# Optimization experiments

Measured on AMD Instinct MI355X. Metric: run time of the kernel, lower is better.

The kernel has to match this reference:

```python
import jax, jax.numpy as jnp
import numpy as np

N, E = 100000, 1600000
IN, EDGE_DIM, HID, OUT, HEADS = 128, 16, 32, 32, 2


def _glorot(key, shape, scale=0.1):
    return jax.random.normal(key, shape, dtype=jnp.float32) * scale


def setup_inputs() -> dict:
    key = jax.random.key(0)
    ks = jax.random.split(key, 20)
    HC1 = HEADS * HID
    return {
        "x": jax.random.normal(ks[0], (N, IN), dtype=jnp.float32),
        "edge_index": jax.random.randint(ks[1], (2, E), 0, N, dtype=jnp.int32),
        "edge_attr": jax.random.normal(ks[2], (E, EDGE_DIM), dtype=jnp.float32),
        # layer 1 (heads=HEADS, concat=True)
        "W1l": _glorot(ks[3], (IN, HC1)), "b1l": jnp.zeros((HC1,), jnp.float32),
        "W1r": _glorot(ks[4], (IN, HC1)), "b1r": jnp.zeros((HC1,), jnp.float32),
        "W1e": _glorot(ks[5], (EDGE_DIM, HC1)),
        "att1": _glorot(ks[6], (HEADS, HID)),
        "bias1": jnp.zeros((HC1,), jnp.float32),
        # layer 2 (heads=1, concat=False)
        "W2l": _glorot(ks[7], (HC1, HID)), "b2l": jnp.zeros((HID,), jnp.float32),
        "W2r": _glorot(ks[8], (HC1, HID)), "b2r": jnp.zeros((HID,), jnp.float32),
        "W2e": _glorot(ks[9], (EDGE_DIM, HID)),
        "att2": _glorot(ks[10], (1, HID)),
        "bias2": jnp.zeros((HID,), jnp.float32),
        # final linear
        "Wlin": _glorot(ks[11], (HID, OUT)), "blin": jnp.zeros((OUT,), jnp.float32),
    }


def gatv2_layer(x, src, dst, edge_attr, Wl, bl, Wr, br, We, att, bias, H, C, concat):
    n = x.shape[0]
    xl = (x @ Wl + bl).reshape(n, H, C)   # source transform (lin_l)
    xr = (x @ Wr + br).reshape(n, H, C)   # target transform (lin_r)
    ea = (edge_attr @ We).reshape(-1, H, C)
    m = xl[src] + xr[dst] + ea                       # [E, H, C]
    e = jnp.sum(jax.nn.leaky_relu(m, 0.2) * att, axis=-1)  # [E, H]
    # segment softmax over incoming edges of each destination node
    emax = jax.ops.segment_max(e, dst, num_segments=n)
    emax = jnp.where(jnp.isfinite(emax), emax, 0.0)
    ee = jnp.exp(e - emax[dst])
    denom = jax.ops.segment_sum(ee, dst, num_segments=n)
    alpha = ee / (denom[dst] + 1e-16)                # [E, H]
    out = jax.ops.segment_sum(xl[src] * alpha[..., None], dst, num_segments=n)  # [N, H, C]
    out = out.reshape(n, H * C) if concat else out.mean(axis=1)
    return out + bias


def reference(x, edge_index, edge_attr, W1l, b1l, W1r, b1r, W1e, att1, bias1,
              W2l, b2l, W2r, b2r, W2e, att2, bias2, Wlin, blin):
    src, dst = edge_index[0], edge_index[1]
    h = jax.nn.elu(gatv2_layer(x, src, dst, edge_attr, W1l, b1l, W1r, b1r, W1e,
                               att1, bias1, HEADS, HID, True))
    h = jax.nn.elu(gatv2_layer(h, src, dst, edge_attr, W2l, b2l, W2r, b2r, W2e,
                               att2, bias2, 1, HID, False))
    return h @ Wlin + blin
```

## Files before the change

### kernel.cpp

```cpp
#include <hip/hip_runtime.h>
#include <hip/hip_fp16.h>
#include <cstdint>
#include <cstddef>


typedef _Float16 half8 __attribute__((ext_vector_type(8)));
typedef float f32x4 __attribute__((ext_vector_type(4)));

__global__ void hist_kernel(const int* __restrict__ dst, int* __restrict__ deg, int E) {
    int e = blockIdx.x * blockDim.x + threadIdx.x;
    if (e < E) atomicAdd(&deg[dst[e]], 1);
}

__global__ void scan_part(const int* __restrict__ deg, int* __restrict__ bsum, int n) {
    int tid = threadIdx.x;
    int base = blockIdx.x * 1024 + tid * 4;
    int s = 0;
#pragma unroll
    for (int j = 0; j < 4; ++j) {
        int i = base + j;
        if (i < n) s += deg[i];
    }
#pragma unroll
    for (int off = 1; off < 64; off <<= 1) s += __shfl_xor(s, off, 64);
    __shared__ int ws[4];
    if ((tid & 63) == 0) ws[tid >> 6] = s;
    __syncthreads();
    if (tid == 0) bsum[blockIdx.x] = ws[0] + ws[1] + ws[2] + ws[3];
}

__global__ void scan_mid(int* __restrict__ bsum, int* __restrict__ rowstart, int nb, int n) {
    int tid = threadIdx.x;
    int v = (tid < nb) ? bsum[tid] : 0;
    int incl = v;
#pragma unroll
    for (int off = 1; off < 64; off <<= 1) {
        int t = __shfl_up(incl, off, 64);
        if ((tid & 63) >= off) incl += t;
    }
    __shared__ int w0;
    if (tid == 63) w0 = incl;
    __syncthreads();
    if (tid >= 64) incl += w0;
    if (tid < nb) bsum[tid] = incl - v;
    if (tid == nb - 1) rowstart[n] = incl;
}

__global__ void scan_fin(const int* __restrict__ deg, const int* __restrict__ bsum,
                         int* __restrict__ rowstart, int n) {
    int tid = threadIdx.x;
    int lane = tid & 63, wid = tid >> 6;
    int base = blockIdx.x * 1024 + tid * 4;
    int v[4];
    int s = 0;
#pragma unroll
    for (int j = 0; j < 4; ++j) {
        int i = base + j;
        v[j] = (i < n) ? deg[i] : 0;
        s += v[j];
    }
    int incl = s;
#pragma unroll
    for (int off = 1; off < 64; off <<= 1) {
        int t = __shfl_up(incl, off, 64);
        if (lane >= off) incl += t;
    }
    __shared__ int ws[4];
    if (lane == 63) ws[wid] = incl;
    __syncthreads();
    int wofs = 0;
    for (int w2 = 0; w2 < wid; ++w2) wofs += ws[w2];
    int acc = bsum[blockIdx.x] + wofs + (incl - s);
#pragma unroll
    for (int j = 0; j < 4; ++j) {
        int i = base + j;
        if (i < n) rowstart[i] = acc;
        acc += v[j];
    }
}

template <int K, int Mh>
__device__ void wprep_body(int i, const float* __restrict__ Wl, const float* __restrict__ Wr,
                           __half* __restrict__ Wfrag) {
    constexpr int KS = K / 32;
    if (i >= K * 2 * Mh) return;
    int j = i & 7;
    int lane = (i >> 3) & 63;
    int rest = i >> 9;
    int ks = rest % KS;
    int nt = rest / KS;
    int k = ks * 32 + ((lane >> 4) & 3) * 8 + j;
    int col = nt * 16 + (lane & 15);
    float v = (col < Mh) ? Wl[k * Mh + col] : Wr[k * Mh + (col - Mh)];
    Wfrag[i] = __float2half(v);
}

__global__ void wprep_both(const float* W1l, const float* W1r, __half* Wf1,
                           const float* W2l, const float* W2r, __half* Wf2) {
    int bid = blockIdx.x;
    int tid = threadIdx.x;
    if (bid < 64) wprep_body<128, 64>(bid * 256 + tid, W1l, W1r, Wf1);
    else          wprep_body<64, 32>((bid - 64) * 256 + tid, W2l, W2r, Wf2);
}

template <int K, int Mh, int BM>
__device__ void gemm_body(int bid, __half* xs, const float* __restrict__ x,
                          const __half* __restrict__ Wfrag, const float* __restrict__ bl,
                          const float* __restrict__ br, __half* __restrict__ yl,
                          __half* __restrict__ yr, int n) {
    constexpr int KS = K / 32;
    constexpr int NT = (2 * Mh) / 16;
    constexpr int RW = BM / 64;
    constexpr int LDP = K + 8;
    int tid = threadIdx.x;
    int lane = tid & 63;
    int wave = tid >> 6;
    int node0 = bid * BM;
    constexpr int ITER = (BM * K) / (256 * 4);
#pragma unroll
    for (int it = 0; it < ITER; ++it) {
        int base = (it * 256 + tid) * 4;
        int row = base / K, kk = base % K;
        float4 v = make_float4(0.f, 0.f, 0.f, 0.f);
        if (node0 + row < n) v = *(const float4*)&x[(size_t)(node0 + row) * K + kk];
        __half2* d = (__half2*)&xs[row * LDP + kk];
        d[0] = __float22half2_rn(make_float2(v.x, v.y));
        d[1] = __float22half2_rn(make_float2(v.z, v.w));
    }
    __syncthreads();
    f32x4 acc[RW][NT];
#pragma unroll
    for (int r = 0; r < RW; ++r)
#pragma unroll
        for (int t = 0; t < NT; ++t) {
            f32x4 z = {0.f, 0.f, 0.f, 0.f};
            acc[r][t] = z;
        }
    int r0 = lane & 15, kof = (lane >> 4) * 8;
#pragma unroll
    for (int ks = 0; ks < KS; ++ks) {
        half8 a[RW];
#pragma unroll
        for (int r = 0; r < RW; ++r) {
            int row = (wave * RW + r) * 16 + r0;
            a[r] = *reinterpret_cast<const half8*>(&xs[row * LDP + ks * 32 + kof]);
        }
#pragma unroll
        for (int t = 0; t < NT; ++t) {
            half8 b = *reinterpret_cast<const half8*>(&Wfrag[(((size_t)t * KS + ks) * 64 + lane) * 8]);
#pragma unroll
            for (int r = 0; r < RW; ++r)
                acc[r][t] = __builtin_amdgcn_mfma_f32_16x16x32_f16(a[r], b, acc[r][t], 0, 0, 0);
        }
    }
#pragma unroll
    for (int r = 0; r < RW; ++r) {
#pragma unroll
        for (int t = 0; t < NT; ++t) {
            int col = t * 16 + (lane & 15);
            float bv = (col < Mh) ? bl[col] : br[col - Mh];
#pragma unroll
            for (int q = 0; q < 4; ++q) {
                int node = node0 + (wave * RW + r) * 16 + (lane >> 4) * 4 + q;
                if (node < n) {
                    float v = acc[r][t][q] + bv;
                    if (col < Mh) yl[(size_t)node * Mh + col] = __float2half(v);
                    else          yr[(size_t)node * Mh + (col - Mh)] = __float2half(v);
                }
            }
        }
    }
}

__device__ void scatter_body(int e, const int* __restrict__ src, const int* __restrict__ dst,
                             const float* __restrict__ eattr, const int* __restrict__ rowstart,
                             int* __restrict__ cursor, int2* __restrict__ es,
                             __half* __restrict__ eah, int E) {
    if (e < E) {
        int d = dst[e];
        int p = atomicAdd(&cursor[d], 1);
        es[rowstart[d] + p] = make_int2(e, src[e]);
        const float4* s4 = (const float4*)&eattr[(size_t)e * 16];
        float4 a = s4[0], b = s4[1], c = s4[2], f = s4[3];
        __half2 h[8];
        h[0] = __float22half2_rn(make_float2(a.x, a.y));
        h[1] = __float22half2_rn(make_float2(a.z, a.w));
        h[2] = __float22half2_rn(make_float2(b.x, b.y));
        h[3] = __float22half2_rn(make_float2(b.z, b.w));
        h[4] = __float22half2_rn(make_float2(c.x, c.y));
        h[5] = __float22half2_rn(make_float2(c.z, c.w));
        h[6] = __float22half2_rn(make_float2(f.x, f.y));
        h[7] = __float22half2_rn(make_float2(f.z, f.w));
        int4* o = (int4*)&eah[(size_t)e * 16];
        o[0] = *(int4*)&h[0];
        o[1] = *(int4*)&h[4];
    }
}

__device__ void dcount_body(int bid, int* h, const int* __restrict__ deg,
                            int* __restrict__ counts, int n) {
    int tid = threadIdx.x;
    h[tid] = 0;
    __syncthreads();
    int base = bid * 4096;
#pragma unroll
    for (int j = 0; j < 16; ++j) {
        int i = base + j * 256 + tid;
        if (i < n) {
            int b = deg[i];
            b = (b > 255) ? 255 : b;
            atomicAdd(&h[b], 1);
        }
    }
    __syncthreads();
    counts[bid * 256 + tid] = h[tid];
}

__global__ __launch_bounds__(256) void fat_kernel(
    int nbG, int nbS,
    const float* __restrict__ x, const __half* __restrict__ Wf1,
    const float* __restrict__ b1l, const float* __restrict__ b1r,
    __half* __restrict__ A, __half* __restrict__ B, int n,
    const int* __restrict__ src, const int* __restrict__ dst,
    const float* __restrict__ eattr, const int* __restrict__ rowstart,
    int* __restrict__ cursor, int2* __restrict__ es, __half* __restrict__ eah, int E,
    const int* __restrict__ deg, int* __restrict__ counts) {
    __shared__ __half xs[64 * 136];
    __shared__ int hcnt[256];
    int bid = blockIdx.x;
    if (bid < nbG) {
        gemm_body<128, 64, 64>(bid, xs, x, Wf1, b1l, b1r, A, B, n);
    } else if (bid < nbG + nbS) {
        scatter_body((bid - nbG) * 256 + threadIdx.x, src, dst, eattr, rowstart, cursor, es,
                     eah, E);
    } else {
        dcount_body(bid - nbG - nbS, hcnt, deg, counts, n);
    }
}

__global__ void dbase_kernel(const int* __restrict__ counts, int* __restrict__ base, int nblk) {
    int b = threadIdx.x;
    int tot = 0;
    for (int k = 0; k < nblk; ++k) tot += counts[k * 256 + b];
    __shared__ int ws[4];
    int lane = b & 63, wid = b >> 6;
    int incl = tot;
#pragma unroll
    for (int off = 1; off < 64; off <<= 1) {
        int t = __shfl_up(incl, off, 64);
        if (lane >= off) incl += t;
    }
    if (lane == 63) ws[wid] = incl;
    __syncthreads();
    int wofs = 0;
    for (int w = 0; w < wid; ++w) wofs += ws[w];
    int acc = wofs + incl - tot;
    for (int k = 0; k < nblk; ++k) {
        base[k * 256 + b] = acc;
        acc += counts[k * 256 + b];
    }
}

__global__ __launch_bounds__(256) void dscatter_block(const int* __restrict__ deg,
                                                      const int* __restrict__ base,
                                                      int* __restrict__ nodeperm, int n) {
    __shared__ int h[256];
    int tid = threadIdx.x;
    h[tid] = 0;
    __syncthreads();
    int bbase = blockIdx.x * 4096;
#pragma unroll
    for (int j = 0; j < 16; ++j) {
        int i = bbase + j * 256 + tid;
        if (i < n) {
            int b = deg[i];
            b = (b > 255) ? 255 : b;
            int r = atomicAdd(&h[b], 1);
            nodeperm[base[blockIdx.x * 256 + b] + r] = i;
        }
    }
}

template <int K, int Mh, int BM>
__global__ __launch_bounds__(256) void gemm_mfma(
    const float* __restrict__ x, const __half* __restrict__ Wfrag,
    const float* __restrict__ bl, const float* __restrict__ br,
    __half* __restrict__ yl, __half* __restrict__ yr, int n) {
    __shared__ __half xs[BM * (K + 8)];
    gemm_body<K, Mh, BM>(blockIdx.x, xs, x, Wfrag, bl, br, yl, yr, n);
}

template <int K, int M, int NPB>
__global__ void linear_kernel(const float* __restrict__ x, const float* __restrict__ W,
                              const float* __restrict__ b, float* __restrict__ y, int n) {
    __shared__ float sx[NPB * K];
    int tid = threadIdx.x;
    int node0 = blockIdx.x * NPB;
    for (int i = tid; i < NPB * K; i += NPB * M) {
        int nn = node0 + i / K;
        sx[i] = (nn < n) ? x[(size_t)nn * K + (i % K)] : 0.f;
    }
    __syncthreads();
    int ln = tid / M, m = tid % M;
    int node = node0 + ln;
    if (node >= n) return;
    float acc = b[m];
#pragma unroll
    for (int k = 0; k < K; ++k) acc = fmaf(sx[ln * K + k], W[k * M + m], acc);
    y[(size_t)node * M + m] = acc;
}

template <int H, int C>
__global__ __launch_bounds__(256) void fused_edge_agg(
    const int* __restrict__ rowstart, const int2* __restrict__ es,
    const __half* __restrict__ eah, const int* __restrict__ nodeperm,
    const float* __restrict__ We,
    const float* __restrict__ att,
    const __half* __restrict__ xl, const __half* __restrict__ xr,
    const float* __restrict__ bias, float* __restrict__ out, int n) {
    constexpr int HC = H * C;
    constexpr int LPN = HC / 2;
    constexpr int NPW = 64 / LPN;
    int gt = blockIdx.x * blockDim.x + threadIdx.x;
    int wave = gt >> 6;
    int lane = threadIdx.x & 63;
    int sub = lane / LPN;
    int j = lane % LPN;
    int ch0 = 2 * j;
    int slot = wave * NPW + sub;
    if (slot >= n) return;
    int node = nodeperm[slot];
    __half2 wh[16];
#pragma unroll
    for (int k = 0; k < 16; ++k) wh[k] = __float22half2_rn(*(const float2*)&We[k * HC + ch0]);
    float2 a2 = *(const float2*)&att[ch0];
    float2 xr2 = __half22float2(*(const __half2*)&xr[(size_t)node * HC + ch0]);
    int beg = rowstart[node], end = rowstart[node + 1];
    float denom = 0.f, acc0 = 0.f, acc1 = 0.f;

    auto gemv = [&](const float4& r0, const float4& r1, const __half2& xlh,
                    float& m0, float& m1, float2& xlf) {
        const __half2* h0 = (const __half2*)&r0;
        const __half2* h1 = (const __half2*)&r1;
        __half2 p0 = __hmul2(__low2half2(h0[0]), wh[0]);
        __half2 p1 = __hmul2(__high2half2(h0[0]), wh[1]);
        p0 = __hfma2(__low2half2(h0[1]), wh[2], p0);
        p1 = __hfma2(__high2half2(h0[1]), wh[3], p1);
        p0 = __hfma2(__low2half2(h0[2]), wh[4], p0);
        p1 = __hfma2(__high2half2(h0[2]), wh[5], p1);
        p0 = __hfma2(__low2half2(h0[3]), wh[6], p0);
        p1 = __hfma2(__high2half2(h0[3]), wh[7], p1);
        p0 = __hfma2(__low2half2(h1[0]), wh[8], p0);
        p1 = __hfma2(__high2half2(h1[0]), wh[9], p1);
        p0 = __hfma2(__low2half2(h1[1]), wh[10], p0);
        p1 = __hfma2(__high2half2(h1[1]), wh[11], p1);
        p0 = __hfma2(__low2half2(h1[2]), wh[12], p0);
        p1 = __hfma2(__high2half2(h1[2]), wh[13], p1);
        p0 = __hfma2(__low2half2(h1[3]), wh[14], p0);
        p1 = __hfma2(__high2half2(h1[3]), wh[15], p1);
        float2 mf = __half22float2(__hadd2(p0, p1));
        xlf = __half22float2(xlh);
        m0 = xlf.x + xr2.x + mf.x;
        m1 = xlf.y + xr2.y + mf.y;
    };
    auto logit = [&](float m0, float m1) -> float {
        m0 = (m0 > 0.f) ? m0 : 0.2f * m0;
        m1 = (m1 > 0.f) ? m1 : 0.2f * m1;
        float v = m0 * a2.x + m1 * a2.y;
#pragma unroll
        for (int msk = 1; msk < 16; msk <<= 1) v += __shfl_xor(v, msk, 64);
        return v;
    };

    int pp = beg;
    for (; pp + 2 <= end; pp += 2) {
        int2 ea = es[pp];
        int2 eb = es[pp + 1];
        const float4* qa = (const float4*)&eah[(size_t)ea.x * 16];
        const float4* qb = (const float4*)&eah[(size_t)eb.x * 16];
        float4 r0a = qa[0], r1a = qa[1];
        float4 r0b = qb[0], r1b = qb[1];
        __half2 xh0 = *(const __half2*)&xl[(size_t)ea.y * HC + ch0];
        __half2 xh1 = *(const __half2*)&xl[(size_t)eb.y * HC + ch0];
        float m0a, m1a, m0b, m1b;
        float2 xla, xlb;
        gemv(r0a, r1a, xh0, m0a, m1a, xla);
        gemv(r0b, r1b, xh1, m0b, m1b, xlb);
        float wa = __expf(logit(m0a, m1a));
        float wb = __expf(logit(m0b, m1b));
        denom += wa + wb;
        acc0 = fmaf(xla.x, wa, acc0);
        acc1 = fmaf(xla.y, wa, acc1);
        acc0 = fmaf(xlb.x, wb, acc0);
        acc1 = fmaf(xlb.y, wb, acc1);
    }
    if (pp < end) {
        int2 ea = es[pp];
        const float4* qa = (const float4*)&eah[(size_t)ea.x * 16];
        float4 r0a = qa[0], r1a = qa[1];
        __half2 xh0 = *(const __half2*)&xl[(size_t)ea.y * HC + ch0];
        float m0a, m1a;
        float2 xla;
        gemv(r0a, r1a, xh0, m0a, m1a, xla);
        float wa = __expf(logit(m0a, m1a));
        denom += wa;
        acc0 = fmaf(xla.x, wa, acc0);
        acc1 = fmaf(xla.y, wa, acc1);
    }
    float2 b2 = *(const float2*)&bias[ch0];
    float inv = 1.f / (denom + 1e-16f);
    float o0 = acc0 * inv + b2.x;
    float o1 = acc1 * inv + b2.y;
    o0 = (o0 > 0.f) ? o0 : __expf(o0) - 1.f;
    o1 = (o1 > 0.f) ? o1 : __expf(o1) - 1.f;
    *(float2*)&out[(size_t)node * HC + ch0] = make_float2(o0, o1);
}

extern "C" void kernel_launch(void* const* d_in, const int* in_sizes, int n_in,
                              void* d_out, int out_size, void* d_ws, size_t ws_size,
                              hipStream_t stream) {
    const float* x     = (const float*)d_in[0];
    const int*   eidx  = (const int*)d_in[1];
    const float* eattr = (const float*)d_in[2];
    const float* W1l   = (const float*)d_in[3];
    const float* b1l   = (const float*)d_in[4];
    const float* W1r   = (const float*)d_in[5];
    const float* b1r   = (const float*)d_in[6];
    const float* W1e   = (const float*)d_in[7];
    const float* att1  = (const float*)d_in[8];
    const float* bias1 = (const float*)d_in[9];
    const float* W2l   = (const float*)d_in[10];
    const float* b2l   = (const float*)d_in[11];
    const float* W2r   = (const float*)d_in[12];
    const float* b2r   = (const float*)d_in[13];
    const float* W2e   = (const float*)d_in[14];
    const float* att2  = (const float*)d_in[15];
    const float* bias2 = (const float*)d_in[16];
    const float* Wlin  = (const float*)d_in[17];
    const float* blin  = (const float*)d_in[18];

    const int N = in_sizes[0] / 128;
    const int E = in_sizes[1] / 2;
    const int* src = eidx;
    const int* dst = eidx + E;
    const int NB_DC = (N + 4095) / 4096;

    char* p = (char*)d_ws;
    auto take = [&](size_t bytes) {
        char* r = p;
        p += (bytes + 255) & ~(size_t)255;
        return r;
    };
    int*    deg      = (int*)take((size_t)N * sizeof(int));
    int*    cursor   = (int*)take((size_t)N * sizeof(int));
    char*   zero_end = p;
    int*    rowstart = (int*)take((size_t)(N + 1) * sizeof(int));
    int*    bsum     = (int*)take(256 * sizeof(int));
    int*    counts   = (int*)take((size_t)(NB_DC + 1) * 256 * sizeof(int));
    int*    dbase    = (int*)take((size_t)(NB_DC + 1) * 256 * sizeof(int));
    int*    nodeperm = (int*)take((size_t)N * sizeof(int));
    int2*   es       = (int2*)take((size_t)E * sizeof(int2));
    __half* eah      = (__half*)take((size_t)E * 16 * sizeof(__half));
    __half* A        = (__half*)take((size_t)N * 64 * sizeof(__half));
    __half* B        = (__half*)take((size_t)N * 64 * sizeof(__half));
    float*  Cbuf     = (float*)take((size_t)N * 64 * sizeof(float));
    __half* Wf1      = (__half*)take((size_t)128 * 128 * sizeof(__half));
    __half* Wf2      = (__half*)take((size_t)64 * 64 * sizeof(__half));

    (void)hipMemsetAsync(deg, 0, (size_t)(zero_end - (char*)deg), stream);
    hist_kernel<<<(E + 255) / 256, 256, 0, stream>>>(dst, deg, E);
    {
        int nb = (N + 1023) / 1024;
        scan_part<<<nb, 256, 0, stream>>>(deg, bsum, N);
        scan_mid<<<1, 128, 0, stream>>>(bsum, rowstart, nb, N);
        scan_fin<<<nb, 256, 0, stream>>>(deg, bsum, rowstart, N);
    }
    wprep_both<<<80, 256, 0, stream>>>(W1l, W1r, Wf1, W2l, W2r, Wf2);

    {
        int nbG = (N + 63) / 64;
        int nbS = (E + 255) / 256;
        fat_kernel<<<nbG + nbS + NB_DC, 256, 0, stream>>>(
            nbG, nbS, x, Wf1, b1l, b1r, A, B, N, src, dst, eattr, rowstart, cursor, es, eah, E,
            deg, counts);
    }
    dbase_kernel<<<1, 256, 0, stream>>>(counts, dbase, NB_DC);
    dscatter_block<<<NB_DC, 256, 0, stream>>>(deg, dbase, nodeperm, N);

    {
        long waves = (N + 1) / 2;
        fused_edge_agg<2, 32><<<(int)((waves * 64 + 255) / 256), 256, 0, stream>>>(
            rowstart, es, eah, nodeperm, W1e, att1, A, B, bias1, Cbuf, N);
    }

    gemm_mfma<64, 32, 128><<<(N + 127) / 128, 256, 0, stream>>>(Cbuf, Wf2, b2l, b2r, A, B, N);
    {
        long waves = (N + 3) / 4;
        fused_edge_agg<1, 32><<<(int)((waves * 64 + 255) / 256), 256, 0, stream>>>(
            rowstart, es, eah, nodeperm, W2e, att2, A, B, bias2, Cbuf, N);
    }

    linear_kernel<32, 32, 8><<<(N + 7) / 8, 256, 0, stream>>>(Cbuf, Wlin, blin, (float*)d_out, N);
}
```

Measured before the change: 408.0 us.

## Store intermediate activations in fp16, merge histogram into weight prep, batch scatter

Intermediate layer outputs (Cbuf) become fp16 instead of fp32, so the layer-2 GEMM and the final linear read half the bytes and the GEMM skips its fp32-to-fp16 conversion on load. The degree histogram is folded into the weight-fragment prep kernel, which removes one launch. The histogram and edge-scatter blocks now handle four edges per thread, issuing their loads together before the atomics. The fat kernel also gets a launch-bounds occupancy hint. The cost is extra rounding of the activations to fp16.

```diff
diff --git a/kernel.cpp b/kernel.cpp
--- a/kernel.cpp
+++ b/kernel.cpp
@@ -6,11 +6,6 @@
 
 typedef _Float16 half8 __attribute__((ext_vector_type(8)));
 typedef float f32x4 __attribute__((ext_vector_type(4)));
-
-__global__ void hist_kernel(const int* __restrict__ dst, int* __restrict__ deg, int E) {
-    int e = blockIdx.x * blockDim.x + threadIdx.x;
-    if (e < E) atomicAdd(&deg[dst[e]], 1);
-}
 
 __global__ void scan_part(const int* __restrict__ deg, int* __restrict__ bsum, int n) {
     int tid = threadIdx.x;
@@ -95,16 +90,27 @@
     Wfrag[i] = __float2half(v);
 }
 
-__global__ void wprep_both(const float* W1l, const float* W1r, __half* Wf1,
+__global__ void pre_kernel(int nbH, const int* __restrict__ dst, int* __restrict__ deg, int E,
+                           const float* W1l, const float* W1r, __half* Wf1,
                            const float* W2l, const float* W2r, __half* Wf2) {
     int bid = blockIdx.x;
     int tid = threadIdx.x;
-    if (bid < 64) wprep_body<128, 64>(bid * 256 + tid, W1l, W1r, Wf1);
-    else          wprep_body<64, 32>((bid - 64) * 256 + tid, W2l, W2r, Wf2);
-}
-
-template <int K, int Mh, int BM>
-__device__ void gemm_body(int bid, __half* xs, const float* __restrict__ x,
+    if (bid < nbH) {
+        int e0 = bid * 1024 + tid;
+#pragma unroll
+        for (int j = 0; j < 4; ++j) {
+            int e = e0 + j * 256;
+            if (e < E) atomicAdd(&deg[dst[e]], 1);
+        }
+    } else {
+        int wb = bid - nbH;
+        if (wb < 64) wprep_body<128, 64>(wb * 256 + tid, W1l, W1r, Wf1);
+        else         wprep_body<64, 32>((wb - 64) * 256 + tid, W2l, W2r, Wf2);
+    }
+}
+
+template <int K, int Mh, int BM, bool HALFIN>
+__device__ void gemm_body(int bid, __half* xs, const void* xin,
                           const __half* __restrict__ Wfrag, const float* __restrict__ bl,
                           const float* __restrict__ br, __half* __restrict__ yl,
                           __half* __restrict__ yr, int n) {
@@ -116,16 +122,30 @@
     int lane = tid & 63;
     int wave = tid >> 6;
     int node0 = bid * BM;
-    constexpr int ITER = (BM * K) / (256 * 4);
-#pragma unroll
-    for (int it = 0; it < ITER; ++it) {
-        int base = (it * 256 + tid) * 4;
-        int row = base / K, kk = base % K;
-        float4 v = make_float4(0.f, 0.f, 0.f, 0.f);
-        if (node0 + row < n) v = *(const float4*)&x[(size_t)(node0 + row) * K + kk];
-        __half2* d = (__half2*)&xs[row * LDP + kk];
-        d[0] = __float22half2_rn(make_float2(v.x, v.y));
-        d[1] = __float22half2_rn(make_float2(v.z, v.w));
+    if constexpr (!HALFIN) {
+        const float* x = (const float*)xin;
+        constexpr int ITER = (BM * K) / (256 * 4);
+#pragma unroll
+        for (int it = 0; it < ITER; ++it) {
+            int base = (it * 256 + tid) * 4;
+            int row = base / K, kk = base % K;
+            float4 v = make_float4(0.f, 0.f, 0.f, 0.f);
+            if (node0 + row < n) v = *(const float4*)&x[(size_t)(node0 + row) * K + kk];
+            __half2* d = (__half2*)&xs[row * LDP + kk];
+            d[0] = __float22half2_rn(make_float2(v.x, v.y));
+            d[1] = __float22half2_rn(make_float2(v.z, v.w));
+        }
+    } else {
+        const __half* x = (const __half*)xin;
+        constexpr int ITER = (BM * K) / (256 * 8);
+#pragma unroll
+        for (int it = 0; it < ITER; ++it) {
+            int base = (it * 256 + tid) * 8;
+            int row = base / K, kk = base % K;
+            int4 v = make_int4(0, 0, 0, 0);
+            if (node0 + row < n) v = *(const int4*)&x[(size_t)(node0 + row) * K + kk];
+            *(int4*)&xs[row * LDP + kk] = v;
+        }
     }
     __syncthreads();
     f32x4 acc[RW][NT];
@@ -172,28 +192,50 @@
     }
 }
 
-__device__ void scatter_body(int e, const int* __restrict__ src, const int* __restrict__ dst,
-                             const float* __restrict__ eattr, const int* __restrict__ rowstart,
-                             int* __restrict__ cursor, int2* __restrict__ es,
-                             __half* __restrict__ eah, int E) {
-    if (e < E) {
-        int d = dst[e];
-        int p = atomicAdd(&cursor[d], 1);
-        es[rowstart[d] + p] = make_int2(e, src[e]);
-        const float4* s4 = (const float4*)&eattr[(size_t)e * 16];
+__device__ void scatter_body4(int e0, const int* __restrict__ src, const int* __restrict__ dst,
+                              const float* __restrict__ eattr, const int* __restrict__ rowstart,
+                              int* __restrict__ cursor, int2* __restrict__ es,
+                              __half* __restrict__ eah, int E) {
+    int e[4], ec[4], d[4], s[4];
+    bool v[4];
+#pragma unroll
+    for (int j = 0; j < 4; ++j) {
+        e[j] = e0 + j * 256;
+        v[j] = e[j] < E;
+        ec[j] = v[j] ? e[j] : (E - 1);
+    }
+#pragma unroll
+    for (int j = 0; j < 4; ++j) {
+        d[j] = dst[ec[j]];
+        s[j] = src[ec[j]];
+    }
+    __half2 hh[4][8];
+#pragma unroll
+    for (int j = 0; j < 4; ++j) {
+        const float4* s4 = (const float4*)&eattr[(size_t)ec[j] * 16];
         float4 a = s4[0], b = s4[1], c = s4[2], f = s4[3];
-        __half2 h[8];
-        h[0] = __float22half2_rn(make_float2(a.x, a.y));
-        h[1] = __float22half2_rn(make_float2(a.z, a.w));
-        h[2] = __float22half2_rn(make_float2(b.x, b.y));
-        h[3] = __float22half2_rn(make_float2(b.z, b.w));
-        h[4] = __float22half2_rn(make_float2(c.x, c.y));
-        h[5] = __float22half2_rn(make_float2(c.z, c.w));
-        h[6] = __float22half2_rn(make_float2(f.x, f.y));
-        h[7] = __float22half2_rn(make_float2(f.z, f.w));
-        int4* o = (int4*)&eah[(size_t)e * 16];
-        o[0] = *(int4*)&h[0];
-        o[1] = *(int4*)&h[4];
+        hh[j][0] = __float22half2_rn(make_float2(a.x, a.y));
+        hh[j][1] = __float22half2_rn(make_float2(a.z, a.w));
+        hh[j][2] = __float22half2_rn(make_float2(b.x, b.y));
+        hh[j][3] = __float22half2_rn(make_float2(b.z, b.w));
+        hh[j][4] = __float22half2_rn(make_float2(c.x, c.y));
+        hh[j][5] = __float22half2_rn(make_float2(c.z, c.w));
+        hh[j][6] = __float22half2_rn(make_float2(f.x, f.y));
+        hh[j][7] = __float22half2_rn(make_float2(f.z, f.w));
+    }
+    int pos[4];
+#pragma unroll
+    for (int j = 0; j < 4; ++j) {
+        pos[j] = v[j] ? (rowstart[d[j]] + atomicAdd(&cursor[d[j]], 1)) : 0;
+    }
+#pragma unroll
+    for (int j = 0; j < 4; ++j) {
+        if (v[j]) {
+            es[pos[j]] = make_int2(e[j], s[j]);
+            int4* o = (int4*)&eah[(size_t)e[j] * 16];
+            o[0] = *(int4*)&hh[j][0];
+            o[1] = *(int4*)&hh[j][4];
+        }
     }
 }
 
@@ -216,7 +258,7 @@
     counts[bid * 256 + tid] = h[tid];
 }
 
-__global__ __launch_bounds__(256) void fat_kernel(
+__global__ __launch_bounds__(256, 4) void fat_kernel(
     int nbG, int nbS,
     const float* __restrict__ x, const __half* __restrict__ Wf1,
     const float* __restrict__ b1l, const float* __restrict__ b1r,
@@ -229,10 +271,10 @@
     __shared__ int hcnt[256];
     int bid = blockIdx.x;
     if (bid < nbG) {
-        gemm_body<128, 64, 64>(bid, xs, x, Wf1, b1l, b1r, A, B, n);
+        gemm_body<128, 64, 64, false>(bid, xs, x, Wf1, b1l, b1r, A, B, n);
     } else if (bid < nbG + nbS) {
-        scatter_body((bid - nbG) * 256 + threadIdx.x, src, dst, eattr, rowstart, cursor, es,
-                     eah, E);
+        scatter_body4((bid - nbG) * 1024 + threadIdx.x, src, dst, eattr, rowstart, cursor, es,
+                      eah, E);
     } else {
         dcount_body(bid - nbG - nbS, hcnt, deg, counts, n);
     }
@@ -282,23 +324,23 @@
 }
 
 template <int K, int Mh, int BM>
-__global__ __launch_bounds__(256) void gemm_mfma(
-    const float* __restrict__ x, const __half* __restrict__ Wfrag,
+__global__ __launch_bounds__(256) void gemm_mfma_h(
+    const __half* __restrict__ x, const __half* __restrict__ Wfrag,
     const float* __restrict__ bl, const float* __restrict__ br,
     __half* __restrict__ yl, __half* __restrict__ yr, int n) {
     __shared__ __half xs[BM * (K + 8)];
-    gemm_body<K, Mh, BM>(blockIdx.x, xs, x, Wfrag, bl, br, yl, yr, n);
+    gemm_body<K, Mh, BM, true>(blockIdx.x, xs, x, Wfrag, bl, br, yl, yr, n);
 }
 
 template <int K, int M, int NPB>
-__global__ void linear_kernel(const float* __restrict__ x, const float* __restrict__ W,
+__global__ void linear_kernel(const __half* __restrict__ x, const float* __restrict__ W,
                               const float* __restrict__ b, float* __restrict__ y, int n) {
     __shared__ float sx[NPB * K];
     int tid = threadIdx.x;
     int node0 = blockIdx.x * NPB;
     for (int i = tid; i < NPB * K; i += NPB * M) {
         int nn = node0 + i / K;
-        sx[i] = (nn < n) ? x[(size_t)nn * K + (i % K)] : 0.f;
+        sx[i] = (nn < n) ? __half2float(x[(size_t)nn * K + (i % K)]) : 0.f;
     }
     __syncthreads();
     int ln = tid / M, m = tid % M;
@@ -317,7 +359,7 @@
     const float* __restrict__ We,
     const float* __restrict__ att,
     const __half* __restrict__ xl, const __half* __restrict__ xr,
-    const float* __restrict__ bias, float* __restrict__ out, int n) {
+    const float* __restrict__ bias, __half* __restrict__ out, int n) {
     constexpr int HC = H * C;
     constexpr int LPN = HC / 2;
     constexpr int NPW = 64 / LPN;
@@ -413,7 +455,7 @@
     float o1 = acc1 * inv + b2.y;
     o0 = (o0 > 0.f) ? o0 : __expf(o0) - 1.f;
     o1 = (o1 > 0.f) ? o1 : __expf(o1) - 1.f;
-    *(float2*)&out[(size_t)node * HC + ch0] = make_float2(o0, o1);
+    *(__half2*)&out[(size_t)node * HC + ch0] = __float22half2_rn(make_float2(o0, o1));
 }
 
 extern "C" void kernel_launch(void* const* d_in, const int* in_sizes, int n_in,
@@ -463,23 +505,25 @@
     __half* eah      = (__half*)take((size_t)E * 16 * sizeof(__half));
     __half* A        = (__half*)take((size_t)N * 64 * sizeof(__half));
     __half* B        = (__half*)take((size_t)N * 64 * sizeof(__half));
-    float*  Cbuf     = (float*)take((size_t)N * 64 * sizeof(float));
+    __half* Chalf    = (__half*)take((size_t)N * 64 * sizeof(__half));
     __half* Wf1      = (__half*)take((size_t)128 * 128 * sizeof(__half));
     __half* Wf2      = (__half*)take((size_t)64 * 64 * sizeof(__half));
 
     (void)hipMemsetAsync(deg, 0, (size_t)(zero_end - (char*)deg), stream);
-    hist_kernel<<<(E + 255) / 256, 256, 0, stream>>>(dst, deg, E);
+    {
+        int nbH = (E + 1023) / 1024;
+        pre_kernel<<<nbH + 80, 256, 0, stream>>>(nbH, dst, deg, E, W1l, W1r, Wf1, W2l, W2r, Wf2);
+    }
     {
         int nb = (N + 1023) / 1024;
         scan_part<<<nb, 256, 0, stream>>>(deg, bsum, N);
         scan_mid<<<1, 128, 0, stream>>>(bsum, rowstart, nb, N);
         scan_fin<<<nb, 256, 0, stream>>>(deg, bsum, rowstart, N);
     }
-    wprep_both<<<80, 256, 0, stream>>>(W1l, W1r, Wf1, W2l, W2r, Wf2);
 
     {
         int nbG = (N + 63) / 64;
-        int nbS = (E + 255) / 256;
+        int nbS = (E + 1023) / 1024;
         fat_kernel<<<nbG + nbS + NB_DC, 256, 0, stream>>>(
             nbG, nbS, x, Wf1, b1l, b1r, A, B, N, src, dst, eattr, rowstart, cursor, es, eah, E,
             deg, counts);
@@ -490,15 +534,15 @@
     {
         long waves = (N + 1) / 2;
         fused_edge_agg<2, 32><<<(int)((waves * 64 + 255) / 256), 256, 0, stream>>>(
-            rowstart, es, eah, nodeperm, W1e, att1, A, B, bias1, Cbuf, N);
-    }
-
-    gemm_mfma<64, 32, 128><<<(N + 127) / 128, 256, 0, stream>>>(Cbuf, Wf2, b2l, b2r, A, B, N);
+            rowstart, es, eah, nodeperm, W1e, att1, A, B, bias1, Chalf, N);
+    }
+
+    gemm_mfma_h<64, 32, 128><<<(N + 127) / 128, 256, 0, stream>>>(Chalf, Wf2, b2l, b2r, A, B, N);
     {
         long waves = (N + 3) / 4;
         fused_edge_agg<1, 32><<<(int)((waves * 64 + 255) / 256), 256, 0, stream>>>(
-            rowstart, es, eah, nodeperm, W2e, att2, A, B, bias2, Cbuf, N);
-    }
-
-    linear_kernel<32, 32, 8><<<(N + 7) / 8, 256, 0, stream>>>(Cbuf, Wlin, blin, (float*)d_out, N);
-}
+            rowstart, es, eah, nodeperm, W2e, att2, A, B, bias2, Chalf, N);
+    }
+
+    linear_kernel<32, 32, 8><<<(N + 7) / 8, 256, 0, stream>>>(Chalf, Wlin, blin, (float*)d_out, N);
+}
```

After: 427.0 us. 1.05x slower.
